# Kernel tuning notes

Hardware: AMD Instinct MI355X
Metric: run time of the kernel (lower is better)

## Reference

```python
import jax, jax.numpy as jnp
import numpy as np

DIM = 512
EDIM = 2 * DIM          # edim(=2) * dim
OUT_DIM = 512
KERNEL_SIZE = 4096
B, L = 4, 4096


def setup_inputs() -> dict:
    key = jax.random.key(0)
    k0, k1, k2, k3, k4 = jax.random.split(key, 5)
    embeddings = jax.random.normal(k0, (B, L, DIM), dtype=jnp.float32)
    logit_alpha = jax.random.uniform(k1, (EDIM,), minval=-3.0, maxval=3.0, dtype=jnp.float32)
    logit_delta = jax.random.uniform(k2, (EDIM,), minval=-3.0, maxval=3.0, dtype=jnp.float32)
    # xavier_uniform: U(-a, a), a = sqrt(6/(fan_in+fan_out))
    a_beta = float(np.sqrt(6.0 / (DIM + EDIM)))
    beta = jax.random.uniform(k3, (DIM, EDIM), minval=-a_beta, maxval=a_beta, dtype=jnp.float32)
    a_eta = float(np.sqrt(6.0 / (EDIM + OUT_DIM)))
    eta = jax.random.uniform(k4, (EDIM, OUT_DIM), minval=-a_eta, maxval=a_eta, dtype=jnp.float32)
    return {"embeddings": embeddings, "logit_alpha": logit_alpha,
            "logit_delta": logit_delta, "beta": beta, "eta": eta}


def reference(embeddings, logit_alpha, logit_delta, beta, eta):
    K = KERNEL_SIZE
    Lseq = embeddings.shape[1]
    # data-dependent EMA decay kernel: kernel[e, t] = p_e * q_e^t
    alpha = jax.nn.sigmoid(logit_alpha)[:, None]            # [E, 1]
    delta = jax.nn.sigmoid(logit_delta)[:, None]            # [E, 1]
    p = alpha
    q = 1.0 - alpha * delta
    len_range = jnp.arange(K, dtype=embeddings.dtype)[None, :]   # [1, K]
    kernel = p * jnp.exp(jnp.log(q) * len_range)            # [E, K]

    u = jnp.einsum('bld,de->ble', embeddings, beta)         # [B, L, E]
    u_T = jnp.swapaxes(u, -1, -2)                           # [B, E, L]

    # forward (causal) direction: flip kernel, full conv via FFT, slice at K-1
    kernel_f = jnp.flip(kernel, axis=-1)
    fft_dim = Lseq + K
    fft_dim = 1 << (fft_dim - 1).bit_length()               # next power of 2 (static)
    inp_fft = jnp.fft.rfft(u_T, n=fft_dim, axis=-1)
    ker_fft = jnp.fft.rfft(kernel_f, n=fft_dim, axis=-1)    # [E, fft_dim//2+1]
    out_full = jnp.fft.irfft(inp_fft * ker_fft, n=fft_dim, axis=-1)
    out_T = out_full[..., K - 1:K - 1 + Lseq].astype(embeddings.dtype)  # [B, E, L]

    out = jnp.swapaxes(out_T, -1, -2)                       # [B, L, E]
    return jnp.einsum('ble,eo->blo', out, eta)              # [B, L, out_dim]
```

## Files before the change

### kernel.cpp

```cpp
#include <hip/hip_runtime.h>
#include <hip/hip_bf16.h>

#define DIM      512
#define EDIM     1024
#define OUTD     512
#define BATCH    4
#define LSEQ     4096
#define MROWS    (BATCH * LSEQ)
#define NCHUNK   64
#define CHUNK    (LSEQ / NCHUNK)

typedef __attribute__((ext_vector_type(8))) __bf16 bf16x8;
typedef __attribute__((ext_vector_type(4))) float  f32x4;

static __device__ __forceinline__ ushort f2b(float f) {
    uint x = __float_as_uint(f);
    x += 0x7fff + ((x >> 16) & 1);
    return (ushort)(x >> 16);
}
static __device__ __forceinline__ float b2f(ushort u) {
    return __uint_as_float(((uint)u) << 16);
}
static __device__ __forceinline__ float sigmoidf(float x) {
    return 1.0f / (1.0f + expf(-x));
}

__global__ void prep_cvt_kernel(const float* __restrict__ emb,
                                ushort* __restrict__ a16,
                                const float* __restrict__ beta,
                                const float* __restrict__ eta,
                                const float* __restrict__ la,
                                const float* __restrict__ ld,
                                ushort* __restrict__ betaT,
                                ushort* __restrict__ etaT,
                                float* __restrict__ p,
                                float* __restrict__ q) {
    __shared__ float tf[32][33];
    int blk = blockIdx.x;
    if (blk < 8192) {
        int i = blk * 256 + threadIdx.x;
        float4 v = ((const float4*)emb)[i];
        ushort4 o;
        o.x = f2b(v.x); o.y = f2b(v.y); o.z = f2b(v.z); o.w = f2b(v.w);
        ((ushort4*)a16)[i] = o;
    } else if (blk < 8704) {
        int tile = blk - 8192;
        int tr = tile >> 5, tc = tile & 31;
        int r = threadIdx.x >> 3, c4 = (threadIdx.x & 7) * 4;
        float4 v = *(const float4*)(beta + (size_t)(tr * 32 + r) * EDIM + tc * 32 + c4);
        tf[r][c4 + 0] = v.x; tf[r][c4 + 1] = v.y;
        tf[r][c4 + 2] = v.z; tf[r][c4 + 3] = v.w;
        __syncthreads();
        ushort4 o;
        o.x = f2b(tf[c4 + 0][r]); o.y = f2b(tf[c4 + 1][r]);
        o.z = f2b(tf[c4 + 2][r]); o.w = f2b(tf[c4 + 3][r]);
        *(ushort4*)(betaT + (size_t)(tc * 32 + r) * DIM + tr * 32 + c4) = o;
    } else if (blk < 9216) {
        int tile = blk - 8704;
        int tr = tile >> 4, tc = tile & 15;
        int r = threadIdx.x >> 3, c4 = (threadIdx.x & 7) * 4;
        float4 v = *(const float4*)(eta + (size_t)(tr * 32 + r) * OUTD + tc * 32 + c4);
        tf[r][c4 + 0] = v.x; tf[r][c4 + 1] = v.y;
        tf[r][c4 + 2] = v.z; tf[r][c4 + 3] = v.w;
        __syncthreads();
        ushort4 o;
        o.x = f2b(tf[c4 + 0][r]); o.y = f2b(tf[c4 + 1][r]);
        o.z = f2b(tf[c4 + 2][r]); o.w = f2b(tf[c4 + 3][r]);
        *(ushort4*)(etaT + (size_t)(tc * 32 + r) * EDIM + tr * 32 + c4) = o;
    } else {
        #pragma unroll
        for (int j = 0; j < 4; ++j) {
            int e = threadIdx.x * 4 + j;
            float a = sigmoidf(la[e]);
            float d = sigmoidf(ld[e]);
            p[e] = a;
            q[e] = 1.0f - a * d;
        }
    }
}

#define MFMA_BF16 __builtin_amdgcn_mfma_f32_16x16x32_bf16
template <int KDIM, int NSHIFT, int OUT_BF16, int DO_AGG>
__global__ __launch_bounds__(512, 2) void gemm256(const ushort* __restrict__ A,
                                                  const ushort* __restrict__ Bt,
                                                  void* __restrict__ Cv,
                                                  const float* __restrict__ qv,
                                                  float* __restrict__ aggp,
                                                  int N) {
    extern __shared__ __align__(16) char smem[];
    const int tid  = threadIdx.x;
    const int lane = tid & 63;
    const int wid  = tid >> 6;
    const int wr   = wid >> 2;
    const int wc   = wid & 3;
    const int l15  = lane & 15;
    const int l4   = lane >> 4;

    const int nwg  = gridDim.x;
    const int flat = ((int)blockIdx.x & 7) * (nwg >> 3) + ((int)blockIdx.x >> 3);
    const int rowBase = (flat >> NSHIFT) << 8;
    const int colBase = (flat & ((1 << NSHIFT) - 1)) << 8;

    const int row0  = tid >> 3;
    const int col16 = (tid & 7) ^ (row0 & 7);
    const ushort* gA0 = A  + (size_t)(rowBase + row0) * KDIM + col16 * 8;
    const ushort* gB0 = Bt + (size_t)(colBase + row0) * KDIM + col16 * 8;
    const int ldsOff = tid * 16;

    const int sw   = (l15 & 7) << 4;
    const int aRow = (wr * 128 + l15) * 128;
    const int bRow = 32768 + (wc * 64 + l15) * 128;
    const int a0 = aRow + ((l4 * 16) ^ sw);
    const int a1 = aRow + ((64 + l4 * 16) ^ sw);
    const int b0 = bRow + ((l4 * 16) ^ sw);
    const int b1 = bRow + ((64 + l4 * 16) ^ sw);

    f32x4 acc[8][4] = {};
    bf16x8 af[4][2], bfr[4][2];

    const int NT = KDIM >> 6;

    auto STAGE = [&](int t) {
        const int boff = (t & 1) << 16;
        const size_t koff = (size_t)t * 64;
        #pragma unroll
        for (int i = 0; i < 4; ++i)
            __builtin_amdgcn_global_load_lds(
                (const __attribute__((address_space(1))) void*)(gA0 + (size_t)i * 64 * KDIM + koff),
                (__attribute__((address_space(3))) void*)(smem + boff + i * 8192 + ldsOff),
                16, 0, 0);
        #pragma unroll
        for (int i = 0; i < 4; ++i)
            __builtin_amdgcn_global_load_lds(
                (const __attribute__((address_space(1))) void*)(gB0 + (size_t)i * 64 * KDIM + koff),
                (__attribute__((address_space(3))) void*)(smem + boff + 32768 + i * 8192 + ldsOff),
                16, 0, 0);
    };

    STAGE(0);
    asm volatile("s_waitcnt vmcnt(0)" ::: "memory");
    __builtin_amdgcn_s_barrier();

    for (int t = 0; t < NT; ++t) {
        const char* sm = smem + ((t & 1) << 16);
        if (t + 1 < NT) STAGE(t + 1);
        #pragma unroll
        for (int m = 0; m < 4; ++m) {
            af[m][0] = *(const bf16x8*)(sm + a0 + m * 2048);
            af[m][1] = *(const bf16x8*)(sm + a1 + m * 2048);
        }
        #pragma unroll
        for (int n = 0; n < 2; ++n) {
            bfr[n][0] = *(const bf16x8*)(sm + b0 + n * 2048);
            bfr[n][1] = *(const bf16x8*)(sm + b1 + n * 2048);
        }
        __builtin_amdgcn_s_barrier();
        __builtin_amdgcn_s_setprio(1);
        #pragma unroll
        for (int m = 0; m < 4; ++m)
            #pragma unroll
            for (int n = 0; n < 2; ++n) {
                acc[m][n] = MFMA_BF16(af[m][0], bfr[n][0], acc[m][n], 0, 0, 0);
                acc[m][n] = MFMA_BF16(af[m][1], bfr[n][1], acc[m][n], 0, 0, 0);
            }
        __builtin_amdgcn_s_setprio(0);
        __builtin_amdgcn_s_barrier();
        #pragma unroll
        for (int n = 2; n < 4; ++n) {
            bfr[n][0] = *(const bf16x8*)(sm + b0 + n * 2048);
            bfr[n][1] = *(const bf16x8*)(sm + b1 + n * 2048);
        }
        __builtin_amdgcn_s_barrier();
        __builtin_amdgcn_s_setprio(1);
        #pragma unroll
        for (int m = 0; m < 4; ++m)
            #pragma unroll
            for (int n = 2; n < 4; ++n) {
                acc[m][n] = MFMA_BF16(af[m][0], bfr[n][0], acc[m][n], 0, 0, 0);
                acc[m][n] = MFMA_BF16(af[m][1], bfr[n][1], acc[m][n], 0, 0, 0);
            }
        __builtin_amdgcn_s_setprio(0);
        __builtin_amdgcn_s_barrier();
        #pragma unroll
        for (int m = 0; m < 4; ++m) {
            af[m][0] = *(const bf16x8*)(sm + a0 + (m + 4) * 2048);
            af[m][1] = *(const bf16x8*)(sm + a1 + (m + 4) * 2048);
        }
        __builtin_amdgcn_s_barrier();
        __builtin_amdgcn_s_setprio(1);
        #pragma unroll
        for (int m = 0; m < 4; ++m)
            #pragma unroll
            for (int n = 0; n < 2; ++n) {
                acc[m + 4][n] = MFMA_BF16(af[m][0], bfr[n][0], acc[m + 4][n], 0, 0, 0);
                acc[m + 4][n] = MFMA_BF16(af[m][1], bfr[n][1], acc[m + 4][n], 0, 0, 0);
            }
        __builtin_amdgcn_s_setprio(0);
        __builtin_amdgcn_s_barrier();
        __builtin_amdgcn_s_setprio(1);
        #pragma unroll
        for (int m = 0; m < 4; ++m)
            #pragma unroll
            for (int n = 2; n < 4; ++n) {
                acc[m + 4][n] = MFMA_BF16(af[m][0], bfr[n][0], acc[m + 4][n], 0, 0, 0);
                acc[m + 4][n] = MFMA_BF16(af[m][1], bfr[n][1], acc[m + 4][n], 0, 0, 0);
            }
        __builtin_amdgcn_s_setprio(0);
        asm volatile("s_waitcnt vmcnt(0)" ::: "memory");
        __builtin_amdgcn_s_barrier();
    }

    #pragma unroll
    for (int m = 0; m < 8; ++m)
        #pragma unroll
        for (int n = 0; n < 4; ++n)
            #pragma unroll
            for (int r = 0; r < 4; ++r) {
                int row = rowBase + wr * 128 + m * 16 + l4 * 4 + r;
                int col = colBase + wc * 64 + n * 16 + l15;
                if (OUT_BF16)
                    ((ushort*)Cv)[(size_t)row * N + col] = f2b(acc[m][n][r]);
                else
                    ((float*)Cv)[(size_t)row * N + col] = acc[m][n][r];
            }

    if (DO_AGG) {
        const int bidx = rowBase >> 12;
        const int chunkBase = ((rowBase & 4095) >> 6) + wr * 2;
        #pragma unroll
        for (int h = 0; h < 2; ++h) {
            #pragma unroll
            for (int n = 0; n < 4; ++n) {
                int col = colBase + wc * 64 + n * 16 + l15;
                float qe = qv[col];
                float q2 = qe * qe, q4 = q2 * q2, q8 = q4 * q4, q16 = q8 * q8;
                float P = 0.0f;
                #pragma unroll
                for (int m = 3; m >= 0; --m) {
                    f32x4 a = acc[h * 4 + m][n];
                    float pm = ((a[3] * qe + a[2]) * qe + a[1]) * qe + a[0];
                    P = P * q16 + pm;
                }
                float ql4 = (l4 & 1 ? q4 : 1.0f) * (l4 & 2 ? q8 : 1.0f);
                P *= ql4;
                P += __shfl_xor(P, 16, 64);
                P += __shfl_xor(P, 32, 64);
                if (l4 == 0)
                    aggp[(((bidx << 6) | (chunkBase + h)) << 10) + col] = P;
            }
        }
    }
}

template <int OUT_BF16>
__global__ __launch_bounds__(256) void gemm_bt(const ushort* __restrict__ A,
                                               const ushort* __restrict__ Bt,
                                               void* __restrict__ Cv,
                                               int M, int N, int K,
                                               int ncolShift) {
    __shared__ ushort smem[16384];
    const int tid  = threadIdx.x;
    const int lane = tid & 63;
    const int wid  = tid >> 6;
    const int wr   = wid >> 1, wc = wid & 1;
    const int l15  = lane & 15;
    const int l4   = lane >> 4;

    const int nwg   = gridDim.x;
    const int chunkw = nwg >> 3;
    const int flat  = (blockIdx.x & 7) * chunkw + (blockIdx.x >> 3);
    const int rowBase = (flat >> ncolShift) << 7;
    const int colBase = (flat & ((1 << ncolShift) - 1)) << 7;

    f32x4 acc[4][4] = {};

    const int nkb = K >> 6;
    for (int kb = 0; kb < nkb; ++kb) {
        #pragma unroll
        for (int r = 0; r < 4; ++r) {
            int c     = r * 256 + tid;
            int row   = c >> 3;
            int col16 = (c & 7) ^ (row & 7);
            const ushort* ga = A  + (size_t)(rowBase + row) * K + kb * 64 + col16 * 8;
            __builtin_amdgcn_global_load_lds(
                (const __attribute__((address_space(1))) void*)ga,
                (__attribute__((address_space(3))) void*)((char*)smem + c * 16),
                16, 0, 0);
            const ushort* gb = Bt + (size_t)(colBase + row) * K + kb * 64 + col16 * 8;
            __builtin_amdgcn_global_load_lds(
                (const __attribute__((address_space(1))) void*)gb,
                (__attribute__((address_space(3))) void*)((char*)smem + 16384 + c * 16),
                16, 0, 0);
        }
        __syncthreads();

        #pragma unroll
        for (int kk = 0; kk < 2; ++kk) {
            bf16x8 af[4], bfr[4];
            #pragma unroll
            for (int m = 0; m < 4; ++m) {
                int row   = wr * 64 + m * 16 + l15;
                int kbyte = kk * 64 + l4 * 16;
                int addr  = row * 128 + (kbyte ^ ((row & 7) << 4));
                af[m] = *(const bf16x8*)((const char*)smem + addr);
            }
            #pragma unroll
            for (int n = 0; n < 4; ++n) {
                int row   = wc * 64 + n * 16 + l15;
                int kbyte = kk * 64 + l4 * 16;
                int addr  = 16384 + row * 128 + (kbyte ^ ((row & 7) << 4));
                bfr[n] = *(const bf16x8*)((const char*)smem + addr);
            }
            #pragma unroll
            for (int m = 0; m < 4; ++m)
                #pragma unroll
                for (int n = 0; n < 4; ++n)
                    acc[m][n] = __builtin_amdgcn_mfma_f32_16x16x32_bf16(
                        af[m], bfr[n], acc[m][n], 0, 0, 0);
        }
        __syncthreads();
    }

    #pragma unroll
    for (int m = 0; m < 4; ++m)
        #pragma unroll
        for (int n = 0; n < 4; ++n)
            #pragma unroll
            for (int r = 0; r < 4; ++r) {
                int row = rowBase + wr * 64 + m * 16 + l4 * 4 + r;
                int col = colBase + wc * 64 + n * 16 + l15;
                if (OUT_BF16)
                    ((ushort*)Cv)[(size_t)row * N + col] = f2b(acc[m][n][r]);
                else
                    ((float*)Cv)[(size_t)row * N + col] = acc[m][n][r];
            }
}

__global__ void scan_apply_kernel(ushort* __restrict__ u,
                                  const float* __restrict__ pv,
                                  const float* __restrict__ qv,
                                  const float* __restrict__ agg) {
    int t = blockIdx.x * blockDim.x + threadIdx.x;
    int e0 = (t & 255) * 4;
    int c  = (t >> 8) & 63;
    int b  = t >> 14;
    float4 qe4 = *(const float4*)(qv + e0);
    float4 pe4 = *(const float4*)(pv + e0);
    float qe[4] = {qe4.x, qe4.y, qe4.z, qe4.w};
    float pe[4] = {pe4.x, pe4.y, pe4.z, pe4.w};
    float qL[4], S[4], w[4];
    #pragma unroll
    for (int k = 0; k < 4; ++k) {
        float x = qe[k];
        #pragma unroll
        for (int s = 0; s < 6; ++s) x *= x;
        qL[k] = x; S[k] = 0.0f; w[k] = 1.0f;
    }
    for (int cp = c + 1; cp < NCHUNK; ++cp) {
        float4 a = *(const float4*)(agg + (((b << 6) | cp) << 10) + e0);
        S[0] += w[0] * a.x;  w[0] *= qL[0];
        S[1] += w[1] * a.y;  w[1] *= qL[1];
        S[2] += w[2] * a.z;  w[2] *= qL[2];
        S[3] += w[3] * a.w;  w[3] *= qL[3];
    }
    ushort* up = u + ((size_t)(b * LSEQ + c * CHUNK) << 10) + e0;
    #pragma unroll 4
    for (int j = CHUNK - 1; j >= 0; --j) {
        ushort4 uv = *(ushort4*)(up + (size_t)j * EDIM);
        ushort4 ov;
        S[0] = b2f(uv.x) + qe[0] * S[0];  ov.x = f2b(pe[0] * S[0]);
        S[1] = b2f(uv.y) + qe[1] * S[1];  ov.y = f2b(pe[1] * S[1]);
        S[2] = b2f(uv.z) + qe[2] * S[2];  ov.z = f2b(pe[2] * S[2]);
        S[3] = b2f(uv.w) + qe[3] * S[3];  ov.w = f2b(pe[3] * S[3]);
        *(ushort4*)(up + (size_t)j * EDIM) = ov;
    }
}

extern "C" void kernel_launch(void* const* d_in, const int* in_sizes, int n_in,
                              void* d_out, int out_size, void* d_ws, size_t ws_size,
                              hipStream_t stream) {
    const float* emb  = (const float*)d_in[0];
    const float* la   = (const float*)d_in[1];
    const float* ld   = (const float*)d_in[2];
    const float* beta = (const float*)d_in[3];
    const float* eta  = (const float*)d_in[4];

    char* ws = (char*)d_ws;
    ushort* a16   = (ushort*)(ws);
    ushort* betaT = (ushort*)(ws + 16777216);
    ushort* etaT  = (ushort*)(ws + 17825792);
    ushort* u     = (ushort*)(ws + 18874368);
    float*  p     = (float*) (ws + 52428800);
    float*  q     = (float*) (ws + 52432896);
    float*  agg   = (float*) (ws + 52436992);

    (void)hipFuncSetAttribute((const void*)gemm256<512, 2, 1, 1>,
                              hipFuncAttributeMaxDynamicSharedMemorySize, 131072);

    prep_cvt_kernel<<<dim3(9217), dim3(256), 0, stream>>>(
        emb, a16, beta, eta, la, ld, betaT, etaT, p, q);

    gemm256<512, 2, 1, 1><<<dim3(256), dim3(512), 131072, stream>>>(
        a16, betaT, (void*)u, q, agg, EDIM);

    scan_apply_kernel<<<dim3(256), dim3(256), 0, stream>>>(u, p, q, agg);

    gemm_bt<0><<<dim3((MROWS / 128) * (OUTD / 128)), dim3(256), 0, stream>>>(
        u, etaT, d_out, MROWS, OUTD, EDIM, 2);
}
```

Baseline: 81.40 us.

## Fuse fp32-to-bf16 embedding conversion into first GEMM with 128x128 tiles

```diff
diff --git a/kernel.cpp b/kernel.cpp
--- a/kernel.cpp
+++ b/kernel.cpp
@@ -25,27 +25,18 @@
     return 1.0f / (1.0f + expf(-x));
 }
 
-__global__ void prep_cvt_kernel(const float* __restrict__ emb,
-                                ushort* __restrict__ a16,
-                                const float* __restrict__ beta,
-                                const float* __restrict__ eta,
-                                const float* __restrict__ la,
-                                const float* __restrict__ ld,
-                                ushort* __restrict__ betaT,
-                                ushort* __restrict__ etaT,
-                                float* __restrict__ p,
-                                float* __restrict__ q) {
+__global__ void prep_kernel(const float* __restrict__ beta,
+                            const float* __restrict__ eta,
+                            const float* __restrict__ la,
+                            const float* __restrict__ ld,
+                            ushort* __restrict__ betaT,
+                            ushort* __restrict__ etaT,
+                            float* __restrict__ p,
+                            float* __restrict__ q) {
     __shared__ float tf[32][33];
     int blk = blockIdx.x;
-    if (blk < 8192) {
-        int i = blk * 256 + threadIdx.x;
-        float4 v = ((const float4*)emb)[i];
-        ushort4 o;
-        o.x = f2b(v.x); o.y = f2b(v.y); o.z = f2b(v.z); o.w = f2b(v.w);
-        ((ushort4*)a16)[i] = o;
-    } else if (blk < 8704) {
-        int tile = blk - 8192;
-        int tr = tile >> 5, tc = tile & 31;
+    if (blk < 512) {
+        int tr = blk >> 5, tc = blk & 31;
         int r = threadIdx.x >> 3, c4 = (threadIdx.x & 7) * 4;
         float4 v = *(const float4*)(beta + (size_t)(tr * 32 + r) * EDIM + tc * 32 + c4);
         tf[r][c4 + 0] = v.x; tf[r][c4 + 1] = v.y;
@@ -55,8 +46,8 @@
         o.x = f2b(tf[c4 + 0][r]); o.y = f2b(tf[c4 + 1][r]);
         o.z = f2b(tf[c4 + 2][r]); o.w = f2b(tf[c4 + 3][r]);
         *(ushort4*)(betaT + (size_t)(tc * 32 + r) * DIM + tr * 32 + c4) = o;
-    } else if (blk < 9216) {
-        int tile = blk - 8704;
+    } else if (blk < 1024) {
+        int tile = blk - 512;
         int tr = tile >> 4, tc = tile & 15;
         int r = threadIdx.x >> 3, c4 = (threadIdx.x & 7) * 4;
         float4 v = *(const float4*)(eta + (size_t)(tr * 32 + r) * OUTD + tc * 32 + c4);
@@ -79,175 +70,145 @@
     }
 }
 
-#define MFMA_BF16 __builtin_amdgcn_mfma_f32_16x16x32_bf16
-template <int KDIM, int NSHIFT, int OUT_BF16, int DO_AGG>
-__global__ __launch_bounds__(512, 2) void gemm256(const ushort* __restrict__ A,
-                                                  const ushort* __restrict__ Bt,
-                                                  void* __restrict__ Cv,
-                                                  const float* __restrict__ qv,
-                                                  float* __restrict__ aggp,
-                                                  int N) {
-    extern __shared__ __align__(16) char smem[];
+__global__ __launch_bounds__(256) void gemm_f32a(const float* __restrict__ A,
+                                                 const ushort* __restrict__ Bt,
+                                                 ushort* __restrict__ Cv,
+                                                 const float* __restrict__ qv,
+                                                 float* __restrict__ aggp,
+                                                 int M, int N, int K,
+                                                 int ncolShift) {
+    __shared__ char smem[49152];
     const int tid  = threadIdx.x;
     const int lane = tid & 63;
     const int wid  = tid >> 6;
-    const int wr   = wid >> 2;
-    const int wc   = wid & 3;
+    const int wr   = wid >> 1, wc = wid & 1;
     const int l15  = lane & 15;
     const int l4   = lane >> 4;
 
-    const int nwg  = gridDim.x;
-    const int flat = ((int)blockIdx.x & 7) * (nwg >> 3) + ((int)blockIdx.x >> 3);
-    const int rowBase = (flat >> NSHIFT) << 8;
-    const int colBase = (flat & ((1 << NSHIFT) - 1)) << 8;
-
-    const int row0  = tid >> 3;
-    const int col16 = (tid & 7) ^ (row0 & 7);
-    const ushort* gA0 = A  + (size_t)(rowBase + row0) * KDIM + col16 * 8;
-    const ushort* gB0 = Bt + (size_t)(colBase + row0) * KDIM + col16 * 8;
-    const int ldsOff = tid * 16;
-
-    const int sw   = (l15 & 7) << 4;
-    const int aRow = (wr * 128 + l15) * 128;
-    const int bRow = 32768 + (wc * 64 + l15) * 128;
-    const int a0 = aRow + ((l4 * 16) ^ sw);
-    const int a1 = aRow + ((64 + l4 * 16) ^ sw);
-    const int b0 = bRow + ((l4 * 16) ^ sw);
-    const int b1 = bRow + ((64 + l4 * 16) ^ sw);
-
-    f32x4 acc[8][4] = {};
-    bf16x8 af[4][2], bfr[4][2];
-
-    const int NT = KDIM >> 6;
-
-    auto STAGE = [&](int t) {
-        const int boff = (t & 1) << 16;
-        const size_t koff = (size_t)t * 64;
-        #pragma unroll
-        for (int i = 0; i < 4; ++i)
+    const int nwg   = gridDim.x;
+    const int flat  = (blockIdx.x & 7) * (nwg >> 3) + (blockIdx.x >> 3);
+    const int rowBase = (flat >> ncolShift) << 7;
+    const int colBase = (flat & ((1 << ncolShift) - 1)) << 7;
+
+    f32x4 acc[4][4] = {};
+    float4 aR[4][2];
+
+    const int nkb = K >> 6;
+
+    int crow[4], ccol[4];
+    #pragma unroll
+    for (int r = 0; r < 4; ++r) {
+        int c = r * 256 + tid;
+        crow[r] = c >> 3;
+        ccol[r] = (c & 7) ^ (crow[r] & 7);
+    }
+
+    auto ISSUE_A = [&](int kb) {
+        #pragma unroll
+        for (int r = 0; r < 4; ++r) {
+            const float* ga = A + (size_t)(rowBase + crow[r]) * K + kb * 64 + ccol[r] * 8;
+            aR[r][0] = *(const float4*)ga;
+            aR[r][1] = *(const float4*)(ga + 4);
+        }
+    };
+    auto ISSUE_B = [&](int kb) {
+        char* dst = smem + 16384 + (kb & 1) * 16384;
+        #pragma unroll
+        for (int r = 0; r < 4; ++r) {
+            const ushort* gb = Bt + (size_t)(colBase + crow[r]) * K + kb * 64 + ccol[r] * 8;
             __builtin_amdgcn_global_load_lds(
-                (const __attribute__((address_space(1))) void*)(gA0 + (size_t)i * 64 * KDIM + koff),
-                (__attribute__((address_space(3))) void*)(smem + boff + i * 8192 + ldsOff),
+                (const __attribute__((address_space(1))) void*)gb,
+                (__attribute__((address_space(3))) void*)(dst + (r * 256 + tid) * 16),
                 16, 0, 0);
-        #pragma unroll
-        for (int i = 0; i < 4; ++i)
-            __builtin_amdgcn_global_load_lds(
-                (const __attribute__((address_space(1))) void*)(gB0 + (size_t)i * 64 * KDIM + koff),
-                (__attribute__((address_space(3))) void*)(smem + boff + 32768 + i * 8192 + ldsOff),
-                16, 0, 0);
+        }
     };
-
-    STAGE(0);
-    asm volatile("s_waitcnt vmcnt(0)" ::: "memory");
+    auto WRITE_A = [&]() {
+        #pragma unroll
+        for (int r = 0; r < 4; ++r) {
+            uint4 v;
+            v.x = (uint)f2b(aR[r][0].x) | ((uint)f2b(aR[r][0].y) << 16);
+            v.y = (uint)f2b(aR[r][0].z) | ((uint)f2b(aR[r][0].w) << 16);
+            v.z = (uint)f2b(aR[r][1].x) | ((uint)f2b(aR[r][1].y) << 16);
+            v.w = (uint)f2b(aR[r][1].z) | ((uint)f2b(aR[r][1].w) << 16);
+            *(uint4*)(smem + (r * 256 + tid) * 16) = v;
+        }
+    };
+
+    ISSUE_A(0);
+    ISSUE_B(0);
+    asm volatile("s_waitcnt vmcnt(8)" ::: "memory");
+    WRITE_A();
+    asm volatile("s_waitcnt vmcnt(0) lgkmcnt(0)" ::: "memory");
     __builtin_amdgcn_s_barrier();
 
-    for (int t = 0; t < NT; ++t) {
-        const char* sm = smem + ((t & 1) << 16);
-        if (t + 1 < NT) STAGE(t + 1);
-        #pragma unroll
-        for (int m = 0; m < 4; ++m) {
-            af[m][0] = *(const bf16x8*)(sm + a0 + m * 2048);
-            af[m][1] = *(const bf16x8*)(sm + a1 + m * 2048);
-        }
-        #pragma unroll
-        for (int n = 0; n < 2; ++n) {
-            bfr[n][0] = *(const bf16x8*)(sm + b0 + n * 2048);
-            bfr[n][1] = *(const bf16x8*)(sm + b1 + n * 2048);
+    for (int kb = 0; kb < nkb; ++kb) {
+        const int kn = (kb < nkb - 1) ? kb + 1 : kb;
+        ISSUE_A(kn);
+        ISSUE_B(kn);
+        const char* bbuf = smem + 16384 + (kb & 1) * 16384;
+        #pragma unroll
+        for (int kk = 0; kk < 2; ++kk) {
+            bf16x8 af[4], bfr[4];
+            #pragma unroll
+            for (int m = 0; m < 4; ++m) {
+                int row   = wr * 64 + m * 16 + l15;
+                int kbyte = kk * 64 + l4 * 16;
+                int addr  = row * 128 + (kbyte ^ ((row & 7) << 4));
+                af[m] = *(const bf16x8*)(smem + addr);
+            }
+            #pragma unroll
+            for (int n = 0; n < 4; ++n) {
+                int row   = wc * 64 + n * 16 + l15;
+                int kbyte = kk * 64 + l4 * 16;
+                int addr  = row * 128 + (kbyte ^ ((row & 7) << 4));
+                bfr[n] = *(const bf16x8*)(bbuf + addr);
+            }
+            #pragma unroll
+            for (int m = 0; m < 4; ++m)
+                #pragma unroll
+                for (int n = 0; n < 4; ++n)
+                    acc[m][n] = __builtin_amdgcn_mfma_f32_16x16x32_bf16(
+                        af[m], bfr[n], acc[m][n], 0, 0, 0);
         }
         __builtin_amdgcn_s_barrier();
-        __builtin_amdgcn_s_setprio(1);
-        #pragma unroll
-        for (int m = 0; m < 4; ++m)
-            #pragma unroll
-            for (int n = 0; n < 2; ++n) {
-                acc[m][n] = MFMA_BF16(af[m][0], bfr[n][0], acc[m][n], 0, 0, 0);
-                acc[m][n] = MFMA_BF16(af[m][1], bfr[n][1], acc[m][n], 0, 0, 0);
-            }
-        __builtin_amdgcn_s_setprio(0);
+        asm volatile("s_waitcnt vmcnt(8)" ::: "memory");
+        WRITE_A();
+        asm volatile("s_waitcnt vmcnt(0) lgkmcnt(0)" ::: "memory");
         __builtin_amdgcn_s_barrier();
-        #pragma unroll
-        for (int n = 2; n < 4; ++n) {
-            bfr[n][0] = *(const bf16x8*)(sm + b0 + n * 2048);
-            bfr[n][1] = *(const bf16x8*)(sm + b1 + n * 2048);
-        }
-        __builtin_amdgcn_s_barrier();
-        __builtin_amdgcn_s_setprio(1);
-        #pragma unroll
-        for (int m = 0; m < 4; ++m)
-            #pragma unroll
-            for (int n = 2; n < 4; ++n) {
-                acc[m][n] = MFMA_BF16(af[m][0], bfr[n][0], acc[m][n], 0, 0, 0);
-                acc[m][n] = MFMA_BF16(af[m][1], bfr[n][1], acc[m][n], 0, 0, 0);
-            }
-        __builtin_amdgcn_s_setprio(0);
-        __builtin_amdgcn_s_barrier();
-        #pragma unroll
-        for (int m = 0; m < 4; ++m) {
-            af[m][0] = *(const bf16x8*)(sm + a0 + (m + 4) * 2048);
-            af[m][1] = *(const bf16x8*)(sm + a1 + (m + 4) * 2048);
-        }
-        __builtin_amdgcn_s_barrier();
-        __builtin_amdgcn_s_setprio(1);
-        #pragma unroll
-        for (int m = 0; m < 4; ++m)
-            #pragma unroll
-            for (int n = 0; n < 2; ++n) {
-                acc[m + 4][n] = MFMA_BF16(af[m][0], bfr[n][0], acc[m + 4][n], 0, 0, 0);
-                acc[m + 4][n] = MFMA_BF16(af[m][1], bfr[n][1], acc[m + 4][n], 0, 0, 0);
-            }
-        __builtin_amdgcn_s_setprio(0);
-        __builtin_amdgcn_s_barrier();
-        __builtin_amdgcn_s_setprio(1);
-        #pragma unroll
-        for (int m = 0; m < 4; ++m)
-            #pragma unroll
-            for (int n = 2; n < 4; ++n) {
-                acc[m + 4][n] = MFMA_BF16(af[m][0], bfr[n][0], acc[m + 4][n], 0, 0, 0);
-                acc[m + 4][n] = MFMA_BF16(af[m][1], bfr[n][1], acc[m + 4][n], 0, 0, 0);
-            }
-        __builtin_amdgcn_s_setprio(0);
-        asm volatile("s_waitcnt vmcnt(0)" ::: "memory");
-        __builtin_amdgcn_s_barrier();
     }
 
     #pragma unroll
-    for (int m = 0; m < 8; ++m)
+    for (int m = 0; m < 4; ++m)
         #pragma unroll
         for (int n = 0; n < 4; ++n)
             #pragma unroll
             for (int r = 0; r < 4; ++r) {
-                int row = rowBase + wr * 128 + m * 16 + l4 * 4 + r;
+                int row = rowBase + wr * 64 + m * 16 + l4 * 4 + r;
                 int col = colBase + wc * 64 + n * 16 + l15;
-                if (OUT_BF16)
-                    ((ushort*)Cv)[(size_t)row * N + col] = f2b(acc[m][n][r]);
-                else
-                    ((float*)Cv)[(size_t)row * N + col] = acc[m][n][r];
-            }
-
-    if (DO_AGG) {
-        const int bidx = rowBase >> 12;
-        const int chunkBase = ((rowBase & 4095) >> 6) + wr * 2;
-        #pragma unroll
-        for (int h = 0; h < 2; ++h) {
-            #pragma unroll
-            for (int n = 0; n < 4; ++n) {
-                int col = colBase + wc * 64 + n * 16 + l15;
-                float qe = qv[col];
-                float q2 = qe * qe, q4 = q2 * q2, q8 = q4 * q4, q16 = q8 * q8;
-                float P = 0.0f;
-                #pragma unroll
-                for (int m = 3; m >= 0; --m) {
-                    f32x4 a = acc[h * 4 + m][n];
-                    float pm = ((a[3] * qe + a[2]) * qe + a[1]) * qe + a[0];
-                    P = P * q16 + pm;
-                }
-                float ql4 = (l4 & 1 ? q4 : 1.0f) * (l4 & 2 ? q8 : 1.0f);
-                P *= ql4;
-                P += __shfl_xor(P, 16, 64);
-                P += __shfl_xor(P, 32, 64);
-                if (l4 == 0)
-                    aggp[(((bidx << 6) | (chunkBase + h)) << 10) + col] = P;
-            }
+                Cv[(size_t)row * N + col] = f2b(acc[m][n][r]);
+            }
+
+    {
+        const int bidx     = rowBase >> 12;
+        const int chunkIdx = ((rowBase & 4095) >> 6) + wr;
+        #pragma unroll
+        for (int n = 0; n < 4; ++n) {
+            int col = colBase + wc * 64 + n * 16 + l15;
+            float qe = qv[col];
+            float q2 = qe * qe, q4 = q2 * q2, q8 = q4 * q4, q16 = q8 * q8;
+            float P = 0.0f;
+            #pragma unroll
+            for (int m = 3; m >= 0; --m) {
+                f32x4 a = acc[m][n];
+                float pm = ((a[3] * qe + a[2]) * qe + a[1]) * qe + a[0];
+                P = P * q16 + pm;
+            }
+            float ql4 = (l4 & 1 ? q4 : 1.0f) * (l4 & 2 ? q8 : 1.0f);
+            P *= ql4;
+            P += __shfl_xor(P, 16, 64);
+            P += __shfl_xor(P, 32, 64);
+            if (l4 == 0)
+                aggp[(((bidx << 6) | chunkIdx) << 10) + col] = P;
         }
     }
 }
@@ -386,22 +347,18 @@
     const float* eta  = (const float*)d_in[4];
 
     char* ws = (char*)d_ws;
-    ushort* a16   = (ushort*)(ws);
-    ushort* betaT = (ushort*)(ws + 16777216);
-    ushort* etaT  = (ushort*)(ws + 17825792);
-    ushort* u     = (ushort*)(ws + 18874368);
-    float*  p     = (float*) (ws + 52428800);
-    float*  q     = (float*) (ws + 52432896);
-    float*  agg   = (float*) (ws + 52436992);
-
-    (void)hipFuncSetAttribute((const void*)gemm256<512, 2, 1, 1>,
-                              hipFuncAttributeMaxDynamicSharedMemorySize, 131072);
-
-    prep_cvt_kernel<<<dim3(9217), dim3(256), 0, stream>>>(
-        emb, a16, beta, eta, la, ld, betaT, etaT, p, q);
-
-    gemm256<512, 2, 1, 1><<<dim3(256), dim3(512), 131072, stream>>>(
-        a16, betaT, (void*)u, q, agg, EDIM);
+    ushort* betaT = (ushort*)(ws);
+    ushort* etaT  = (ushort*)(ws + 1048576);
+    ushort* u     = (ushort*)(ws + 2097152);
+    float*  p     = (float*) (ws + 35651584);
+    float*  q     = (float*) (ws + 35655680);
+    float*  agg   = (float*) (ws + 35659776);
+
+    prep_kernel<<<dim3(1025), dim3(256), 0, stream>>>(beta, eta, la, ld,
+                                                      betaT, etaT, p, q);
+
+    gemm_f32a<<<dim3((MROWS / 128) * (EDIM / 128)), dim3(256), 0, stream>>>(
+        emb, betaT, u, q, agg, MROWS, EDIM, DIM, 3);
 
     scan_apply_kernel<<<dim3(256), dim3(256), 0, stream>>>(u, p, q, agg);
 
```

Result: slower. 95.14 us (+16.9%).

## Fuse chunked EMA scan into first GEMM via cooperative grid sync

Applied to the files above, without the earlier changes.

```diff
diff --git a/kernel.cpp b/kernel.cpp
--- a/kernel.cpp
+++ b/kernel.cpp
@@ -1,5 +1,8 @@
 #include <hip/hip_runtime.h>
 #include <hip/hip_bf16.h>
+#include <hip/hip_cooperative_groups.h>
+
+namespace cg = cooperative_groups;
 
 #define DIM      512
 #define EDIM     1024
@@ -7,8 +10,6 @@
 #define BATCH    4
 #define LSEQ     4096
 #define MROWS    (BATCH * LSEQ)
-#define NCHUNK   64
-#define CHUNK    (LSEQ / NCHUNK)
 
 typedef __attribute__((ext_vector_type(8))) __bf16 bf16x8;
 typedef __attribute__((ext_vector_type(4))) float  f32x4;
@@ -17,9 +18,6 @@
     uint x = __float_as_uint(f);
     x += 0x7fff + ((x >> 16) & 1);
     return (ushort)(x >> 16);
-}
-static __device__ __forceinline__ float b2f(ushort u) {
-    return __uint_as_float(((uint)u) << 16);
 }
 static __device__ __forceinline__ float sigmoidf(float x) {
     return 1.0f / (1.0f + expf(-x));
@@ -80,13 +78,11 @@
 }
 
 #define MFMA_BF16 __builtin_amdgcn_mfma_f32_16x16x32_bf16
-template <int KDIM, int NSHIFT, int OUT_BF16, int DO_AGG>
-__global__ __launch_bounds__(512, 2) void gemm256(const ushort* __restrict__ A,
-                                                  const ushort* __restrict__ Bt,
-                                                  void* __restrict__ Cv,
-                                                  const float* __restrict__ qv,
-                                                  float* __restrict__ aggp,
-                                                  int N) {
+
+__global__ __launch_bounds__(512, 1) void gemm1_coop(
+        const ushort* __restrict__ A, const ushort* __restrict__ Bt,
+        ushort* __restrict__ Cv, const float* __restrict__ qv,
+        const float* __restrict__ pv, float* __restrict__ aggp) {
     extern __shared__ __align__(16) char smem[];
     const int tid  = threadIdx.x;
     const int lane = tid & 63;
@@ -98,13 +94,13 @@
 
     const int nwg  = gridDim.x;
     const int flat = ((int)blockIdx.x & 7) * (nwg >> 3) + ((int)blockIdx.x >> 3);
-    const int rowBase = (flat >> NSHIFT) << 8;
-    const int colBase = (flat & ((1 << NSHIFT) - 1)) << 8;
+    const int rowBase = (flat >> 2) << 8;
+    const int colBase = (flat & 3) << 8;
 
     const int row0  = tid >> 3;
     const int col16 = (tid & 7) ^ (row0 & 7);
-    const ushort* gA0 = A  + (size_t)(rowBase + row0) * KDIM + col16 * 8;
-    const ushort* gB0 = Bt + (size_t)(colBase + row0) * KDIM + col16 * 8;
+    const ushort* gA0 = A  + (size_t)(rowBase + row0) * DIM + col16 * 8;
+    const ushort* gB0 = Bt + (size_t)(colBase + row0) * DIM + col16 * 8;
     const int ldsOff = tid * 16;
 
     const int sw   = (l15 & 7) << 4;
@@ -118,7 +114,7 @@
     f32x4 acc[8][4] = {};
     bf16x8 af[4][2], bfr[4][2];
 
-    const int NT = KDIM >> 6;
+    const int NT = DIM >> 6;
 
     auto STAGE = [&](int t) {
         const int boff = (t & 1) << 16;
@@ -126,13 +122,13 @@
         #pragma unroll
         for (int i = 0; i < 4; ++i)
             __builtin_amdgcn_global_load_lds(
-                (const __attribute__((address_space(1))) void*)(gA0 + (size_t)i * 64 * KDIM + koff),
+                (const __attribute__((address_space(1))) void*)(gA0 + (size_t)i * 64 * DIM + koff),
                 (__attribute__((address_space(3))) void*)(smem + boff + i * 8192 + ldsOff),
                 16, 0, 0);
         #pragma unroll
         for (int i = 0; i < 4; ++i)
             __builtin_amdgcn_global_load_lds(
-                (const __attribute__((address_space(1))) void*)(gB0 + (size_t)i * 64 * KDIM + koff),
+                (const __attribute__((address_space(1))) void*)(gB0 + (size_t)i * 64 * DIM + koff),
                 (__attribute__((address_space(3))) void*)(smem + boff + 32768 + i * 8192 + ldsOff),
                 16, 0, 0);
     };
@@ -210,43 +206,82 @@
         __builtin_amdgcn_s_barrier();
     }
 
+    const int bidx      = rowBase >> 12;
+    const int chunkBase = ((rowBase & 4095) >> 6) + wr * 2;
+
+    float Bv[2][4][4];
     #pragma unroll
-    for (int m = 0; m < 8; ++m)
-        #pragma unroll
-        for (int n = 0; n < 4; ++n)
-            #pragma unroll
-            for (int r = 0; r < 4; ++r) {
-                int row = rowBase + wr * 128 + m * 16 + l4 * 4 + r;
-                int col = colBase + wc * 64 + n * 16 + l15;
-                if (OUT_BF16)
-                    ((ushort*)Cv)[(size_t)row * N + col] = f2b(acc[m][n][r]);
-                else
-                    ((float*)Cv)[(size_t)row * N + col] = acc[m][n][r];
-            }
-
-    if (DO_AGG) {
-        const int bidx = rowBase >> 12;
-        const int chunkBase = ((rowBase & 4095) >> 6) + wr * 2;
+    for (int h = 0; h < 2; ++h) {
+        #pragma unroll
+        for (int n = 0; n < 4; ++n) {
+            int col = colBase + wc * 64 + n * 16 + l15;
+            float qe = qv[col];
+            float q2 = qe * qe, q4 = q2 * q2, q8 = q4 * q4, q16 = q8 * q8;
+            float ql4 = (l4 & 1 ? q4 : 1.0f) * (l4 & 2 ? q8 : 1.0f);
+            #pragma unroll
+            for (int g = 0; g < 4; ++g) {
+                f32x4 a = acc[h * 4 + g][n];
+                float seg = ((a[3] * qe + a[2]) * qe + a[1]) * qe + a[0];
+                float v = seg * ql4;
+                v += __shfl_xor(v, 16, 64);
+                v += __shfl_xor(v, 32, 64);
+                Bv[h][n][g] = v;
+            }
+            float aggv = ((Bv[h][n][3] * q16 + Bv[h][n][2]) * q16
+                          + Bv[h][n][1]) * q16 + Bv[h][n][0];
+            if (l4 == 0)
+                aggp[(((bidx << 6) | (chunkBase + h)) << 10) + col] = aggv;
+        }
+    }
+    __threadfence();
+    cg::this_grid().sync();
+
+    #pragma unroll
+    for (int n = 0; n < 4; ++n) {
+        int col = colBase + wc * 64 + n * 16 + l15;
+        float qe = qv[col], pe = pv[col];
+        float q2 = qe * qe, q4 = q2 * q2, q8 = q4 * q4, q16 = q8 * q8;
+        float q12 = q4 * q8;
+        float qL = q16 * q16; qL = qL * qL;
+        float carry1 = 0.0f;
+        for (int cp = 63; cp >= chunkBase + 2; --cp)
+            carry1 = aggp[(((bidx << 6) | cp) << 10) + col] + qL * carry1;
+        float carry0 = aggp[(((bidx << 6) | (chunkBase + 1)) << 10) + col]
+                       + qL * carry1;
         #pragma unroll
         for (int h = 0; h < 2; ++h) {
-            #pragma unroll
-            for (int n = 0; n < 4; ++n) {
-                int col = colBase + wc * 64 + n * 16 + l15;
-                float qe = qv[col];
-                float q2 = qe * qe, q4 = q2 * q2, q8 = q4 * q4, q16 = q8 * q8;
-                float P = 0.0f;
-                #pragma unroll
-                for (int m = 3; m >= 0; --m) {
-                    f32x4 a = acc[h * 4 + m][n];
-                    float pm = ((a[3] * qe + a[2]) * qe + a[1]) * qe + a[0];
-                    P = P * q16 + pm;
-                }
-                float ql4 = (l4 & 1 ? q4 : 1.0f) * (l4 & 2 ? q8 : 1.0f);
-                P *= ql4;
-                P += __shfl_xor(P, 16, 64);
-                P += __shfl_xor(P, 32, 64);
-                if (l4 == 0)
-                    aggp[(((bidx << 6) | (chunkBase + h)) << 10) + col] = P;
+            float carry = h ? carry1 : carry0;
+            float Tn[4];
+            Tn[3] = carry;
+            Tn[2] = Bv[h][n][3] + q16 * Tn[3];
+            Tn[1] = Bv[h][n][2] + q16 * Tn[2];
+            Tn[0] = Bv[h][n][1] + q16 * Tn[1];
+            #pragma unroll
+            for (int g = 0; g < 4; ++g) {
+                f32x4 a = acc[h * 4 + g][n];
+                float seg = ((a[3] * qe + a[2]) * qe + a[1]) * qe + a[0];
+                float s16 = __shfl(seg, lane + 16, 64);
+                float s32 = __shfl(seg, lane + 32, 64);
+                float s48 = __shfl(seg, lane + 48, 64);
+                float suf = seg
+                          + (l4 <= 2 ? q4  * s16 : 0.0f)
+                          + (l4 <= 1 ? q8  * s32 : 0.0f)
+                          + (l4 == 0 ? q12 * s48 : 0.0f);
+                float fac = (l4 == 0) ? q16 : (l4 == 1) ? q12
+                          : (l4 == 2) ? q8  : q4;
+                float S0 = suf + fac * Tn[g];
+                float Sn4 = __shfl(S0, lane + 16, 64);
+                if (l4 == 3) Sn4 = Tn[g];
+                float S3 = a[3] + qe * Sn4;
+                float S2 = a[2] + qe * S3;
+                float S1 = a[1] + qe * S2;
+                float S0b = a[0] + qe * S1;
+                int row = rowBase + wr * 128 + (h * 4 + g) * 16 + l4 * 4;
+                ushort* dst = Cv + (size_t)row * EDIM + col;
+                dst[0 * EDIM] = f2b(pe * S0b);
+                dst[1 * EDIM] = f2b(pe * S1);
+                dst[2 * EDIM] = f2b(pe * S2);
+                dst[3 * EDIM] = f2b(pe * S3);
             }
         }
     }
@@ -336,46 +371,6 @@
             }
 }
 
-__global__ void scan_apply_kernel(ushort* __restrict__ u,
-                                  const float* __restrict__ pv,
-                                  const float* __restrict__ qv,
-                                  const float* __restrict__ agg) {
-    int t = blockIdx.x * blockDim.x + threadIdx.x;
-    int e0 = (t & 255) * 4;
-    int c  = (t >> 8) & 63;
-    int b  = t >> 14;
-    float4 qe4 = *(const float4*)(qv + e0);
-    float4 pe4 = *(const float4*)(pv + e0);
-    float qe[4] = {qe4.x, qe4.y, qe4.z, qe4.w};
-    float pe[4] = {pe4.x, pe4.y, pe4.z, pe4.w};
-    float qL[4], S[4], w[4];
-    #pragma unroll
-    for (int k = 0; k < 4; ++k) {
-        float x = qe[k];
-        #pragma unroll
-        for (int s = 0; s < 6; ++s) x *= x;
-        qL[k] = x; S[k] = 0.0f; w[k] = 1.0f;
-    }
-    for (int cp = c + 1; cp < NCHUNK; ++cp) {
-        float4 a = *(const float4*)(agg + (((b << 6) | cp) << 10) + e0);
-        S[0] += w[0] * a.x;  w[0] *= qL[0];
-        S[1] += w[1] * a.y;  w[1] *= qL[1];
-        S[2] += w[2] * a.z;  w[2] *= qL[2];
-        S[3] += w[3] * a.w;  w[3] *= qL[3];
-    }
-    ushort* up = u + ((size_t)(b * LSEQ + c * CHUNK) << 10) + e0;
-    #pragma unroll 4
-    for (int j = CHUNK - 1; j >= 0; --j) {
-        ushort4 uv = *(ushort4*)(up + (size_t)j * EDIM);
-        ushort4 ov;
-        S[0] = b2f(uv.x) + qe[0] * S[0];  ov.x = f2b(pe[0] * S[0]);
-        S[1] = b2f(uv.y) + qe[1] * S[1];  ov.y = f2b(pe[1] * S[1]);
-        S[2] = b2f(uv.z) + qe[2] * S[2];  ov.z = f2b(pe[2] * S[2]);
-        S[3] = b2f(uv.w) + qe[3] * S[3];  ov.w = f2b(pe[3] * S[3]);
-        *(ushort4*)(up + (size_t)j * EDIM) = ov;
-    }
-}
-
 extern "C" void kernel_launch(void* const* d_in, const int* in_sizes, int n_in,
                               void* d_out, int out_size, void* d_ws, size_t ws_size,
                               hipStream_t stream) {
@@ -394,16 +389,21 @@
     float*  q     = (float*) (ws + 52432896);
     float*  agg   = (float*) (ws + 52436992);
 
-    (void)hipFuncSetAttribute((const void*)gemm256<512, 2, 1, 1>,
+    (void)hipFuncSetAttribute((const void*)gemm1_coop,
                               hipFuncAttributeMaxDynamicSharedMemorySize, 131072);
 
     prep_cvt_kernel<<<dim3(9217), dim3(256), 0, stream>>>(
         emb, a16, beta, eta, la, ld, betaT, etaT, p, q);
 
-    gemm256<512, 2, 1, 1><<<dim3(256), dim3(512), 131072, stream>>>(
-        a16, betaT, (void*)u, q, agg, EDIM);
-
-    scan_apply_kernel<<<dim3(256), dim3(256), 0, stream>>>(u, p, q, agg);
+    {
+        const ushort* A_ = a16; const ushort* B_ = betaT; ushort* C_ = u;
+        const float* q_ = q; const float* p_ = p; float* g_ = agg;
+        void* args[] = { (void*)&A_, (void*)&B_, (void*)&C_,
+                         (void*)&q_, (void*)&p_, (void*)&g_ };
+        (void)hipLaunchCooperativeKernel((const void*)gemm1_coop,
+                                         dim3(256), dim3(512),
+                                         args, 131072, stream);
+    }
 
     gemm_bt<0><<<dim3((MROWS / 128) * (OUTD / 128)), dim3(256), 0, stream>>>(
         u, etaT, d_out, MROWS, OUTD, EDIM, 2);
```

After: 182.6 us. 2.24x slower.
